# Kernel tuning notes

Measured on AMD Instinct MI355X. Metric: run time of the kernel, lower is better.

The kernel has to match this reference:

```python
import jax, jax.numpy as jnp
import numpy as np

FEAT_DIM = 256
HEAD_DIM = 32
N_HEADS = FEAT_DIM // HEAD_DIM
SIZE = 8  # sqrt(max_seq_len)
P = SIZE * SIZE  # 64
B, G = 4, 1024


def _rel_pos_index(size: int) -> np.ndarray:
    coords = np.stack(np.meshgrid(np.arange(size), np.arange(size), indexing='ij'))
    flat = coords.reshape(2, -1)
    rel = flat[:, :, None] - flat[:, None, :]
    rel = rel.transpose(1, 2, 0).copy()
    rel[:, :, 0] += size - 1
    rel[:, :, 1] += size - 1
    rel[:, :, 0] *= 2 * size - 1
    return rel.sum(-1)  # [P, P], values in [0, (2*size-1)^2)


def setup_inputs() -> dict:
    key = jax.random.key(0)
    ks = jax.random.split(key, 6)
    d = FEAT_DIM
    w_std = d ** -0.5
    return {
        'x': jax.random.normal(ks[0], (B, G, P, d), dtype=jnp.float32),
        'Wqkv': jax.random.normal(ks[1], (d, 3 * d), dtype=jnp.float32) * w_std,
        'bqkv': jnp.zeros((3 * d,), dtype=jnp.float32),
        'Wm': jax.random.normal(ks[2], (d, d), dtype=jnp.float32) * w_std,
        'bm': jnp.zeros((d,), dtype=jnp.float32),
        'bias_table': jax.random.normal(ks[3], ((2 * SIZE - 1) ** 2, N_HEADS), dtype=jnp.float32) * 0.02,
        'rel_index': jnp.asarray(_rel_pos_index(SIZE), dtype=jnp.int32),
    }


def reference(x, Wqkv, bqkv, Wm, bm, bias_table, rel_index):
    Bb, Gg, Pp, D = x.shape
    H, DH = N_HEADS, HEAD_DIM
    scale = D ** -0.5  # note: scale uses feat_dim, as in the original
    qkv = x @ Wqkv + bqkv  # [B,G,P,3D]
    q, k, v = jnp.split(qkv, 3, axis=-1)
    q = q.reshape(Bb, Gg, Pp, H, DH)
    k = k.reshape(Bb, Gg, Pp, H, DH) * scale
    v = v.reshape(Bb, Gg, Pp, H, DH)
    scores = jnp.einsum('BGIHD,BGJHD->BGHIJ', q, k)  # [B,G,H,P,P]
    # gathered relative-position bias: [P,P,H] -> [1,1,H,P,P]
    bias = bias_table[rel_index]  # [P,P,H]
    bias = jnp.transpose(bias, (2, 0, 1))[None, None]  # [1,1,H,P,P]
    attn = jax.nn.softmax(scores + bias, axis=-1)
    out = jnp.einsum('BGHIJ,BGJHD->BGIHD', attn, v)
    out = out.reshape(Bb, Gg, Pp, D)
    return out @ Wm + bm
```

## Files before the change

kernel.cpp:

```cpp
#include <hip/hip_runtime.h>
#include <hip/hip_bf16.h>

typedef short short8 __attribute__((ext_vector_type(8)));
typedef float f32x4 __attribute__((ext_vector_type(4)));

#define XB_OFF 0
#define SCR_OFF 16896
#define LDS_TOT 37376
#define STX 264
#define ST40 40
#define ST72 72

static __device__ __forceinline__ unsigned short f2b(float f) {
  union { float f; unsigned u; } v; v.f = f;
  unsigned r = v.u + 0x7FFFu + ((v.u >> 16) & 1u);
  return (unsigned short)(r >> 16);
}
static __device__ __forceinline__ unsigned pk2(float a, float b) {
  union { __hip_bfloat162 h; unsigned u; } v;
  v.h = __float22bfloat162_rn(make_float2(a, b));
  return v.u;
}

__global__ void prep_w_kernel(const float* __restrict__ W, unsigned short* __restrict__ Wf,
                              int ncols, int total, int qkv) {
  const int tid = blockIdx.x * blockDim.x + threadIdx.x;
  if (tid >= total) return;
  const int l  = tid & 63;
  const int ks = (tid >> 6) & 7;
  const int nt = tid >> 9;
  int col; float scl = 1.0f;
  if (qkv) {
    const int wv = nt / 6, tt = nt % 6;
    col = (tt >> 1) * 256 + wv * 32 + (tt & 1) * 16 + (l & 15);
    if ((tt >> 1) == 1) scl = 0.0625f;
  } else {
    col = nt * 16 + (l & 15);
  }
  const int k0 = ks * 32 + (l >> 4) * 8;
  short8 v;
#pragma unroll
  for (int j = 0; j < 8; ++j) v[j] = (short)f2b(W[(size_t)(k0 + j) * ncols + col] * scl);
  *reinterpret_cast<short8*>(&Wf[(size_t)tid * 8]) = v;
}

__global__ void prep_bias_kernel(const float* __restrict__ bt, const int* __restrict__ ri,
                                 float* __restrict__ bc) {
  const int tid = blockIdx.x * blockDim.x + threadIdx.x;
  if (tid >= 8192) return;
  const int l  = tid & 63;
  const int t  = (tid >> 6) & 15;
  const int h  = tid >> 10;
  const int mt = t >> 2, nt = t & 3;
  f32x4 v;
#pragma unroll
  for (int i = 0; i < 4; ++i) {
    const int r = mt * 16 + (l >> 4) * 4 + i;
    const int c = nt * 16 + (l & 15);
    v[i] = bt[ri[r * 64 + c] * 8 + h];
  }
  *reinterpret_cast<f32x4*>(&bc[(size_t)tid * 4]) = v;
}

__global__ __launch_bounds__(512, 4)
void win_attn_kernel(const float* __restrict__ x,
                     const float* __restrict__ bqkv,
                     const float* __restrict__ bm,
                     const unsigned short* __restrict__ Wqkv_f,
                     const unsigned short* __restrict__ Wm_f,
                     const float* __restrict__ bias_c,
                     float* __restrict__ out)
{
  __shared__ unsigned short sm[LDS_TOT];
  const int tid = threadIdx.x;
  const int w   = tid >> 6;
  const int l   = tid & 63;
  const int lr  = l & 15;
  const int lg  = l >> 4;
  const long long win = blockIdx.x;
  const float* xw = x + win * 16384;
  const int SW = SCR_OFF + w * 2560;

#pragma unroll
  for (int it = 0; it < 8; ++it) {
    const int f = it * 2048 + tid * 4;
    const int row = f >> 8, col = f & 255;
    const float4 v = *reinterpret_cast<const float4*>(xw + f);
    *reinterpret_cast<uint2*>(&sm[XB_OFF + row * STX + col]) =
        make_uint2(pk2(v.x, v.y), pk2(v.z, v.w));
  }
  __syncthreads();

  short8 qf[4], kf[4], vf[2][2];
#pragma unroll
  for (int m = 0; m < 3; ++m) {
    f32x4 acc[4][2];
    {
      float bb0 = bqkv[m * 256 + w * 32 + lr];
      float bb1 = bqkv[m * 256 + w * 32 + 16 + lr];
      if (m == 1) { bb0 *= 0.0625f; bb1 *= 0.0625f; }
#pragma unroll
      for (int mt = 0; mt < 4; ++mt) {
        acc[mt][0] = (f32x4){bb0, bb0, bb0, bb0};
        acc[mt][1] = (f32x4){bb1, bb1, bb1, bb1};
      }
    }
#pragma unroll
    for (int ks = 0; ks < 8; ++ks) {
      short8 a[4];
#pragma unroll
      for (int mt = 0; mt < 4; ++mt)
        a[mt] = *reinterpret_cast<const short8*>(
            &sm[XB_OFF + (lr + 16 * mt) * STX + lg * 8 + ks * 32]);
#pragma unroll
      for (int sub = 0; sub < 2; ++sub) {
        const short8 bf = *reinterpret_cast<const short8*>(
            &Wqkv_f[(size_t)(((w * 6 + m * 2 + sub) * 8 + ks) * 64 + l) * 8]);
#pragma unroll
        for (int mt = 0; mt < 4; ++mt)
          acc[mt][sub] = __builtin_amdgcn_mfma_f32_16x16x32_bf16(a[mt], bf, acc[mt][sub], 0, 0, 0);
      }
    }

    if (m == 2) {
#pragma unroll
      for (int sub = 0; sub < 2; ++sub)
#pragma unroll
        for (int mt = 0; mt < 4; ++mt)
          *reinterpret_cast<uint2*>(&sm[SW + (sub * 16 + lr) * ST72 + 16 * mt + 4 * lg]) =
              make_uint2(pk2(acc[mt][sub][0], acc[mt][sub][1]),
                         pk2(acc[mt][sub][2], acc[mt][sub][3]));
#pragma unroll
      for (int nt = 0; nt < 2; ++nt)
#pragma unroll
        for (int kh = 0; kh < 2; ++kh)
          vf[nt][kh] = *reinterpret_cast<const short8*>(
              &sm[SW + (lr + 16 * nt) * ST72 + kh * 32 + lg * 8]);
    } else {
#pragma unroll
      for (int sub = 0; sub < 2; ++sub)
#pragma unroll
        for (int mt = 0; mt < 4; ++mt) {
          const unsigned p01 = pk2(acc[mt][sub][0], acc[mt][sub][1]);
          const unsigned p23 = pk2(acc[mt][sub][2], acc[mt][sub][3]);
          const int b = SW + (16 * mt + 4 * lg) * ST40 + sub * 16 + lr;
          sm[b]            = (unsigned short)p01;
          sm[b + ST40]     = (unsigned short)(p01 >> 16);
          sm[b + 2 * ST40] = (unsigned short)p23;
          sm[b + 3 * ST40] = (unsigned short)(p23 >> 16);
        }
#pragma unroll
      for (int mt = 0; mt < 4; ++mt) {
        const short8 fr = *reinterpret_cast<const short8*>(
            &sm[SW + (lr + 16 * mt) * ST40 + lg * 8]);
        if (m == 0) qf[mt] = fr; else kf[mt] = fr;
      }
    }
  }

  f32x4 s[4][4];
#pragma unroll
  for (int mt = 0; mt < 4; ++mt)
#pragma unroll
    for (int nt = 0; nt < 4; ++nt) {
      const f32x4 bb = *reinterpret_cast<const f32x4*>(
          &bias_c[(size_t)((w * 16 + mt * 4 + nt) * 64 + l) * 4]);
      s[mt][nt] = __builtin_amdgcn_mfma_f32_16x16x32_bf16(qf[mt], kf[nt], bb, 0, 0, 0);
    }
  float rinv[4][4];
#pragma unroll
  for (int mt = 0; mt < 4; ++mt)
#pragma unroll
    for (int i = 0; i < 4; ++i) {
      float mx = fmaxf(fmaxf(s[mt][0][i], s[mt][1][i]), fmaxf(s[mt][2][i], s[mt][3][i]));
      mx = fmaxf(mx, __shfl_xor(mx, 1));
      mx = fmaxf(mx, __shfl_xor(mx, 2));
      mx = fmaxf(mx, __shfl_xor(mx, 4));
      mx = fmaxf(mx, __shfl_xor(mx, 8));
      const float e0 = __expf(s[mt][0][i] - mx);
      const float e1 = __expf(s[mt][1][i] - mx);
      const float e2 = __expf(s[mt][2][i] - mx);
      const float e3 = __expf(s[mt][3][i] - mx);
      float sum = e0 + e1 + e2 + e3;
      sum += __shfl_xor(sum, 1);
      sum += __shfl_xor(sum, 2);
      sum += __shfl_xor(sum, 4);
      sum += __shfl_xor(sum, 8);
      rinv[mt][i] = 1.0f / sum;
      s[mt][0][i] = e0; s[mt][1][i] = e1; s[mt][2][i] = e2; s[mt][3][i] = e3;
    }

  f32x4 o[4][2];
#pragma unroll
  for (int mt = 0; mt < 4; ++mt)
#pragma unroll
    for (int nt = 0; nt < 2; ++nt) o[mt][nt] = (f32x4){0.f, 0.f, 0.f, 0.f};
#pragma unroll
  for (int kh = 0; kh < 2; ++kh) {
#pragma unroll
    for (int ntl = 0; ntl < 2; ++ntl)
#pragma unroll
      for (int mt = 0; mt < 4; ++mt) {
        const int nt = 2 * kh + ntl;
        const unsigned p01 = pk2(s[mt][nt][0], s[mt][nt][1]);
        const unsigned p23 = pk2(s[mt][nt][2], s[mt][nt][3]);
        const int b = SW + (16 * mt + 4 * lg) * ST40 + ntl * 16 + lr;
        sm[b]            = (unsigned short)p01;
        sm[b + ST40]     = (unsigned short)(p01 >> 16);
        sm[b + 2 * ST40] = (unsigned short)p23;
        sm[b + 3 * ST40] = (unsigned short)(p23 >> 16);
      }
#pragma unroll
    for (int mt = 0; mt < 4; ++mt) {
      const short8 pa = *reinterpret_cast<const short8*>(
          &sm[SW + (lr + 16 * mt) * ST40 + lg * 8]);
#pragma unroll
      for (int nt = 0; nt < 2; ++nt)
        o[mt][nt] = __builtin_amdgcn_mfma_f32_16x16x32_bf16(pa, vf[nt][kh], o[mt][nt], 0, 0, 0);
    }
  }

  __syncthreads();
#pragma unroll
  for (int mt = 0; mt < 4; ++mt)
#pragma unroll
    for (int nt = 0; nt < 2; ++nt) {
      const unsigned p01 = pk2(o[mt][nt][0] * rinv[mt][0], o[mt][nt][1] * rinv[mt][1]);
      const unsigned p23 = pk2(o[mt][nt][2] * rinv[mt][2], o[mt][nt][3] * rinv[mt][3]);
      const int b = XB_OFF + (16 * mt + 4 * lg) * STX + w * 32 + nt * 16 + lr;
      sm[b]           = (unsigned short)p01;
      sm[b + STX]     = (unsigned short)(p01 >> 16);
      sm[b + 2 * STX] = (unsigned short)p23;
      sm[b + 3 * STX] = (unsigned short)(p23 >> 16);
    }
  __syncthreads();

  f32x4 po[2][4];
#pragma unroll
  for (int mt = 0; mt < 2; ++mt) {
    const f32x4 bi = *reinterpret_cast<const f32x4*>(&bm[w * 32 + mt * 16 + 4 * lg]);
#pragma unroll
    for (int nt = 0; nt < 4; ++nt) po[mt][nt] = bi;
  }
#pragma unroll
  for (int ks = 0; ks < 8; ++ks) {
    short8 bx[4];
#pragma unroll
    for (int nt = 0; nt < 4; ++nt)
      bx[nt] = *reinterpret_cast<const short8*>(
          &sm[XB_OFF + (lr + 16 * nt) * STX + lg * 8 + ks * 32]);
#pragma unroll
    for (int mt = 0; mt < 2; ++mt) {
      const short8 af = *reinterpret_cast<const short8*>(
          &Wm_f[(size_t)(((w * 2 + mt) * 8 + ks) * 64 + l) * 8]);
#pragma unroll
      for (int nt = 0; nt < 4; ++nt)
        po[mt][nt] = __builtin_amdgcn_mfma_f32_16x16x32_bf16(af, bx[nt], po[mt][nt], 0, 0, 0);
    }
  }
  float* ow = out + win * 16384;
#pragma unroll
  for (int mt = 0; mt < 2; ++mt)
#pragma unroll
    for (int nt = 0; nt < 4; ++nt)
      *reinterpret_cast<f32x4*>(&ow[(lr + 16 * nt) * 256 + w * 32 + mt * 16 + 4 * lg]) = po[mt][nt];
}

extern "C" void kernel_launch(void* const* d_in, const int* in_sizes, int n_in,
                              void* d_out, int out_size, void* d_ws, size_t ws_size,
                              hipStream_t stream) {
  const float* x    = (const float*)d_in[0];
  const float* Wqkv = (const float*)d_in[1];
  const float* bqkv = (const float*)d_in[2];
  const float* Wm   = (const float*)d_in[3];
  const float* bm   = (const float*)d_in[4];
  const float* bt   = (const float*)d_in[5];
  const int*   ri   = (const int*)d_in[6];

  unsigned short* Wqkv_f = (unsigned short*)d_ws;
  unsigned short* Wm_f   = (unsigned short*)((char*)d_ws + 393216);
  float*          bias_c = (float*)((char*)d_ws + 524288);

  prep_w_kernel<<<48, 512, 0, stream>>>(Wqkv, Wqkv_f, 768, 24576, 1);
  prep_w_kernel<<<16, 512, 0, stream>>>(Wm, Wm_f, 256, 8192, 0);
  prep_bias_kernel<<<16, 512, 0, stream>>>(bt, ri, bias_c);

  const int nwin = in_sizes[0] / 16384;
  win_attn_kernel<<<nwin, 512, 0, stream>>>(x, bqkv, bm, Wqkv_f, Wm_f, bias_c, (float*)d_out);
}
```

Measured before the change: 286.3 us.

## Halve per-wave LDS scratch and swap output projection operand roles

Each wave's scratch region is halved by staging Q/K/V tiles and probability tiles in two half-passes through a 40-stride buffer instead of one full 72-stride buffer. This cuts total LDS per block, and launch bounds are raised from 4 to 6 blocks per CU to raise occupancy. The output projection now uses the activation as the A operand and the weights as B, so bias is broadcast per column and stores become scalar per element instead of float4. The higher block count may force register spilling, and the scalar output stores may reduce write efficiency.

```diff
diff --git a/kernel.cpp b/kernel.cpp
--- a/kernel.cpp
+++ b/kernel.cpp
@@ -6,10 +6,9 @@
 
 #define XB_OFF 0
 #define SCR_OFF 16896
-#define LDS_TOT 37376
+#define LDS_TOT 27136
 #define STX 264
 #define ST40 40
-#define ST72 72
 
 static __device__ __forceinline__ unsigned short f2b(float f) {
   union { float f; unsigned u; } v; v.f = f;
@@ -62,7 +61,7 @@
   *reinterpret_cast<f32x4*>(&bc[(size_t)tid * 4]) = v;
 }
 
-__global__ __launch_bounds__(512, 4)
+__global__ __launch_bounds__(512, 6)
 void win_attn_kernel(const float* __restrict__ x,
                      const float* __restrict__ bqkv,
                      const float* __restrict__ bm,
@@ -79,7 +78,7 @@
   const int lg  = l >> 4;
   const long long win = blockIdx.x;
   const float* xw = x + win * 16384;
-  const int SW = SCR_OFF + w * 2560;
+  const int SW = SCR_OFF + w * 1280;
 
 #pragma unroll
   for (int it = 0; it < 8; ++it) {
@@ -124,36 +123,43 @@
 
     if (m == 2) {
 #pragma unroll
-      for (int sub = 0; sub < 2; ++sub)
-#pragma unroll
-        for (int mt = 0; mt < 4; ++mt)
-          *reinterpret_cast<uint2*>(&sm[SW + (sub * 16 + lr) * ST72 + 16 * mt + 4 * lg]) =
-              make_uint2(pk2(acc[mt][sub][0], acc[mt][sub][1]),
-                         pk2(acc[mt][sub][2], acc[mt][sub][3]));
-#pragma unroll
-      for (int nt = 0; nt < 2; ++nt)
-#pragma unroll
-        for (int kh = 0; kh < 2; ++kh)
+      for (int kh = 0; kh < 2; ++kh) {
+#pragma unroll
+        for (int sub = 0; sub < 2; ++sub)
+#pragma unroll
+          for (int mtl = 0; mtl < 2; ++mtl) {
+            const int mt = 2 * kh + mtl;
+            *reinterpret_cast<uint2*>(&sm[SW + (sub * 16 + lr) * ST40 + 16 * mtl + 4 * lg]) =
+                make_uint2(pk2(acc[mt][sub][0], acc[mt][sub][1]),
+                           pk2(acc[mt][sub][2], acc[mt][sub][3]));
+          }
+#pragma unroll
+        for (int nt = 0; nt < 2; ++nt)
           vf[nt][kh] = *reinterpret_cast<const short8*>(
-              &sm[SW + (lr + 16 * nt) * ST72 + kh * 32 + lg * 8]);
+              &sm[SW + (lr + 16 * nt) * ST40 + lg * 8]);
+      }
     } else {
 #pragma unroll
-      for (int sub = 0; sub < 2; ++sub)
-#pragma unroll
-        for (int mt = 0; mt < 4; ++mt) {
-          const unsigned p01 = pk2(acc[mt][sub][0], acc[mt][sub][1]);
-          const unsigned p23 = pk2(acc[mt][sub][2], acc[mt][sub][3]);
-          const int b = SW + (16 * mt + 4 * lg) * ST40 + sub * 16 + lr;
-          sm[b]            = (unsigned short)p01;
-          sm[b + ST40]     = (unsigned short)(p01 >> 16);
-          sm[b + 2 * ST40] = (unsigned short)p23;
-          sm[b + 3 * ST40] = (unsigned short)(p23 >> 16);
+      for (int th = 0; th < 2; ++th) {
+#pragma unroll
+        for (int sub = 0; sub < 2; ++sub)
+#pragma unroll
+          for (int mtl = 0; mtl < 2; ++mtl) {
+            const int mt = 2 * th + mtl;
+            const unsigned p01 = pk2(acc[mt][sub][0], acc[mt][sub][1]);
+            const unsigned p23 = pk2(acc[mt][sub][2], acc[mt][sub][3]);
+            const int b = SW + (16 * mtl + 4 * lg) * ST40 + sub * 16 + lr;
+            sm[b]            = (unsigned short)p01;
+            sm[b + ST40]     = (unsigned short)(p01 >> 16);
+            sm[b + 2 * ST40] = (unsigned short)p23;
+            sm[b + 3 * ST40] = (unsigned short)(p23 >> 16);
+          }
+#pragma unroll
+        for (int tl = 0; tl < 2; ++tl) {
+          const short8 fr = *reinterpret_cast<const short8*>(
+              &sm[SW + (lr + 16 * tl) * ST40 + lg * 8]);
+          if (m == 0) qf[2 * th + tl] = fr; else kf[2 * th + tl] = fr;
         }
-#pragma unroll
-      for (int mt = 0; mt < 4; ++mt) {
-        const short8 fr = *reinterpret_cast<const short8*>(
-            &sm[SW + (lr + 16 * mt) * ST40 + lg * 8]);
-        if (m == 0) qf[mt] = fr; else kf[mt] = fr;
       }
     }
   }
@@ -198,25 +204,29 @@
 #pragma unroll
   for (int kh = 0; kh < 2; ++kh) {
 #pragma unroll
-    for (int ntl = 0; ntl < 2; ++ntl)
-#pragma unroll
-      for (int mt = 0; mt < 4; ++mt) {
-        const int nt = 2 * kh + ntl;
-        const unsigned p01 = pk2(s[mt][nt][0], s[mt][nt][1]);
-        const unsigned p23 = pk2(s[mt][nt][2], s[mt][nt][3]);
-        const int b = SW + (16 * mt + 4 * lg) * ST40 + ntl * 16 + lr;
-        sm[b]            = (unsigned short)p01;
-        sm[b + ST40]     = (unsigned short)(p01 >> 16);
-        sm[b + 2 * ST40] = (unsigned short)p23;
-        sm[b + 3 * ST40] = (unsigned short)(p23 >> 16);
-      }
-#pragma unroll
-    for (int mt = 0; mt < 4; ++mt) {
-      const short8 pa = *reinterpret_cast<const short8*>(
-          &sm[SW + (lr + 16 * mt) * ST40 + lg * 8]);
-#pragma unroll
-      for (int nt = 0; nt < 2; ++nt)
-        o[mt][nt] = __builtin_amdgcn_mfma_f32_16x16x32_bf16(pa, vf[nt][kh], o[mt][nt], 0, 0, 0);
+    for (int th = 0; th < 2; ++th) {
+#pragma unroll
+      for (int ntl = 0; ntl < 2; ++ntl)
+#pragma unroll
+        for (int mtl = 0; mtl < 2; ++mtl) {
+          const int mt = 2 * th + mtl, nt = 2 * kh + ntl;
+          const unsigned p01 = pk2(s[mt][nt][0], s[mt][nt][1]);
+          const unsigned p23 = pk2(s[mt][nt][2], s[mt][nt][3]);
+          const int b = SW + (16 * mtl + 4 * lg) * ST40 + ntl * 16 + lr;
+          sm[b]            = (unsigned short)p01;
+          sm[b + ST40]     = (unsigned short)(p01 >> 16);
+          sm[b + 2 * ST40] = (unsigned short)p23;
+          sm[b + 3 * ST40] = (unsigned short)(p23 >> 16);
+        }
+#pragma unroll
+      for (int tl = 0; tl < 2; ++tl) {
+        const int mt = 2 * th + tl;
+        const short8 pa = *reinterpret_cast<const short8*>(
+            &sm[SW + (lr + 16 * tl) * ST40 + lg * 8]);
+#pragma unroll
+        for (int nt = 0; nt < 2; ++nt)
+          o[mt][nt] = __builtin_amdgcn_mfma_f32_16x16x32_bf16(pa, vf[nt][kh], o[mt][nt], 0, 0, 0);
+      }
     }
   }
 
@@ -235,35 +245,41 @@
     }
   __syncthreads();
 
-  f32x4 po[2][4];
-#pragma unroll
-  for (int mt = 0; mt < 2; ++mt) {
-    const f32x4 bi = *reinterpret_cast<const f32x4*>(&bm[w * 32 + mt * 16 + 4 * lg]);
-#pragma unroll
-    for (int nt = 0; nt < 4; ++nt) po[mt][nt] = bi;
+  f32x4 po[4][2];
+  {
+    const float bm0 = bm[w * 32 + lr];
+    const float bm1 = bm[w * 32 + 16 + lr];
+#pragma unroll
+    for (int mt = 0; mt < 4; ++mt) {
+      po[mt][0] = (f32x4){bm0, bm0, bm0, bm0};
+      po[mt][1] = (f32x4){bm1, bm1, bm1, bm1};
+    }
   }
 #pragma unroll
   for (int ks = 0; ks < 8; ++ks) {
-    short8 bx[4];
-#pragma unroll
-    for (int nt = 0; nt < 4; ++nt)
-      bx[nt] = *reinterpret_cast<const short8*>(
-          &sm[XB_OFF + (lr + 16 * nt) * STX + lg * 8 + ks * 32]);
-#pragma unroll
-    for (int mt = 0; mt < 2; ++mt) {
-      const short8 af = *reinterpret_cast<const short8*>(
-          &Wm_f[(size_t)(((w * 2 + mt) * 8 + ks) * 64 + l) * 8]);
-#pragma unroll
-      for (int nt = 0; nt < 4; ++nt)
-        po[mt][nt] = __builtin_amdgcn_mfma_f32_16x16x32_bf16(af, bx[nt], po[mt][nt], 0, 0, 0);
-    }
-  }
+    short8 a[4];
+#pragma unroll
+    for (int mt = 0; mt < 4; ++mt)
+      a[mt] = *reinterpret_cast<const short8*>(
+          &sm[XB_OFF + (lr + 16 * mt) * STX + lg * 8 + ks * 32]);
+#pragma unroll
+    for (int nt = 0; nt < 2; ++nt) {
+      const short8 bf = *reinterpret_cast<const short8*>(
+          &Wm_f[(size_t)(((w * 2 + nt) * 8 + ks) * 64 + l) * 8]);
+#pragma unroll
+      for (int mt = 0; mt < 4; ++mt)
+        po[mt][nt] = __builtin_amdgcn_mfma_f32_16x16x32_bf16(a[mt], bf, po[mt][nt], 0, 0, 0);
+    }
+  }
+
   float* ow = out + win * 16384;
 #pragma unroll
-  for (int mt = 0; mt < 2; ++mt)
-#pragma unroll
-    for (int nt = 0; nt < 4; ++nt)
-      *reinterpret_cast<f32x4*>(&ow[(lr + 16 * nt) * 256 + w * 32 + mt * 16 + 4 * lg]) = po[mt][nt];
+  for (int mt = 0; mt < 4; ++mt)
+#pragma unroll
+    for (int nt = 0; nt < 2; ++nt)
+#pragma unroll
+      for (int i = 0; i < 4; ++i)
+        ow[(16 * mt + 4 * lg + i) * 256 + w * 32 + nt * 16 + lr] = po[mt][nt][i];
 }
 
 extern "C" void kernel_launch(void* const* d_in, const int* in_sizes, int n_in,
```

Result: slower. 611.4 us (+113.6%).
